# Optimization experiments

Hardware: AMD Instinct MI355X
Metric: run time of the kernel (lower is better)

The kernel has to match this reference:

```python
import jax, jax.numpy as jnp
import numpy as np
from jax import lax

B, T, C = 8, 1025, 512
HEADS = 8
CACHE = 256          # int(dim * cache_ratio)
CLS = 1
L = 256              # gr_cache memory length
H = W = 32           # sqrt(T - CLS)
EPS = 1e-5


def setup_inputs() -> dict:
    key = jax.random.key(0)
    ks = jax.random.split(key, 40)
    def w(k, shape, scale=0.02):
        return jax.random.normal(k, shape, dtype=jnp.float32) * scale
    inp = {}
    inp['x'] = jax.random.normal(ks[0], (B, T, C), dtype=jnp.float32)
    inp['gr_cache'] = jax.random.normal(ks[1], (1, L, CACHE), dtype=jnp.float32)
    # self-attention (dim=512) params, weights stored (in, out)
    inp['Wq1'] = w(ks[2], (C, C)); inp['bq1'] = jnp.zeros((C,), jnp.float32)
    inp['Wk1'] = w(ks[3], (C, C)); inp['bk1'] = jnp.zeros((C,), jnp.float32)
    inp['Wv1'] = w(ks[4], (C, C)); inp['bv1'] = jnp.zeros((C,), jnp.float32)
    inp['Wo1'] = w(ks[5], (C, C)); inp['bo1'] = jnp.zeros((C,), jnp.float32)
    # memory attention (dim=cache_dim=256) params
    inp['Wq2'] = w(ks[6], (CACHE, CACHE)); inp['bq2'] = jnp.zeros((CACHE,), jnp.float32)
    inp['Wk2'] = w(ks[7], (CACHE, CACHE)); inp['bk2'] = jnp.zeros((CACHE,), jnp.float32)
    inp['Wv2'] = w(ks[8], (CACHE, CACHE)); inp['bv2'] = jnp.zeros((CACHE,), jnp.float32)
    inp['Wo2'] = w(ks[9], (CACHE, CACHE)); inp['bo2'] = jnp.zeros((CACHE,), jnp.float32)
    # GRU-style gate linears: in = 2*cache_dim, out = cache_dim
    inp['Wr'] = w(ks[10], (2 * CACHE, CACHE)); inp['br'] = jnp.zeros((CACHE,), jnp.float32)
    inp['Wz'] = w(ks[11], (2 * CACHE, CACHE)); inp['bz'] = jnp.zeros((CACHE,), jnp.float32)
    inp['Wa'] = w(ks[12], (2 * CACHE, CACHE)); inp['ba'] = jnp.zeros((CACHE,), jnp.float32)
    # LayerNorm(cache_dim)
    inp['gamma'] = jnp.ones((CACHE,), jnp.float32)
    inp['beta'] = jnp.zeros((CACHE,), jnp.float32)
    # per-head gate logits, init to -1 as in the module
    inp['lam'] = jnp.full((HEADS,), -1.0, dtype=jnp.float32)
    # grouped conv pos-emb: Conv2d(512, 512, k=3, groups=CACHE) -> (O=512, I/g=2, 3, 3)
    inp['conv_w'] = w(ks[13], (C, C // CACHE, 3, 3))
    inp['conv_b'] = jnp.zeros((C,), jnp.float32)
    return inp


def _mha(q_in, kv_in, Wq, bq, Wk, bk, Wv, bv, Wo, bo):
    Bq, Tq, D = q_in.shape
    Tk = kv_in.shape[1]
    dh = D // HEADS
    q = (q_in @ Wq + bq).reshape(Bq, Tq, HEADS, dh)
    k = (kv_in @ Wk + bk).reshape(Bq, Tk, HEADS, dh)
    v = (kv_in @ Wv + bv).reshape(Bq, Tk, HEADS, dh)
    s = jnp.einsum('bqhd,bkhd->bhqk', q, k) * (1.0 / np.sqrt(dh)).astype(np.float32)
    a = jax.nn.softmax(s, axis=-1)
    o = jnp.einsum('bhqk,bkhd->bqhd', a, v).reshape(Bq, Tq, D)
    return o @ Wo + bo


def reference(x, gr_cache, Wq1, bq1, Wk1, bk1, Wv1, bv1, Wo1, bo1,
              Wq2, bq2, Wk2, bk2, Wv2, bv2, Wo2, bo2,
              Wr, br, Wz, bz, Wa, ba, gamma, beta, lam, conv_w, conv_b):
    B_, T_, C_ = x.shape
    # ---- spatial positional embedding (faithful to torch view->permute quirk) ----
    tok = x[:, CLS:, :].reshape(B_, H, W, C_).transpose(0, 3, 1, 2)   # (B, C, H, W)
    pos = lax.conv_general_dilated(tok, conv_w, (1, 1), 'SAME',
                                   feature_group_count=CACHE,
                                   dimension_numbers=('NCHW', 'OIHW', 'NCHW'))
    pos = pos + conv_b[None, :, None, None]
    pos = pos.reshape(B_, C_, T_ - CLS).transpose(0, 2, 1)            # (B, T-1, C)
    pos = jnp.concatenate([jnp.zeros((B_, CLS, C_), pos.dtype), pos], axis=1)
    # ---- self attention ----
    x_self = _mha(x, x, Wq1, bq1, Wk1, bk1, Wv1, bv1, Wo1, bo1)       # (B, T, C)
    x_self_h = x_self.reshape(B_, T_, HEADS, C_ // HEADS)
    # ---- GRU-style gated cache update ----
    gr = jnp.broadcast_to(gr_cache, (B_, L, CACHE))
    x_summary = x_self[:, :, :CACHE]
    idx = (jnp.arange(L) * T_) // L                                   # nearest interpolate T -> L
    x_summary = x_summary[:, idx, :]                                  # (B, L, CACHE)
    cat = jnp.concatenate([gr, x_summary], axis=-1)
    reset = jax.nn.sigmoid(cat @ Wr + br)
    z = jax.nn.sigmoid(cat @ Wz + bz)
    cat2 = jnp.concatenate([reset * gr, x_summary], axis=-1)
    add = jax.nn.gelu(cat2 @ Wa + ba, approximate=False)
    mu = add.mean(-1, keepdims=True)
    var = ((add - mu) ** 2).mean(-1, keepdims=True)
    add = (add - mu) / jnp.sqrt(var + EPS) * gamma + beta             # LayerNorm
    gr_new = z * add + (1.0 - z) * gr
    # ---- memory attention on first cache_dim channels ----
    x_mem = _mha(x[:, :, :CACHE], gr_new, Wq2, bq2, Wk2, bk2, Wv2, bv2, Wo2, bo2)
    x_mem = x_mem.reshape(B_, T_, HEADS, CACHE // HEADS)
    # ---- per-head alpha blend with zero-padded mem branch ----
    alpha = jax.nn.sigmoid(lam).reshape(1, 1, HEADS, 1)
    pad = jnp.zeros((B_, T_, HEADS, (C_ - CACHE) // HEADS), x.dtype)
    out = (alpha * jnp.concatenate([x_mem, pad], axis=-1)
           + (1.0 - alpha) * x_self_h).reshape(B_, T_, C_) + pos
    return out
```

## Files before the change

kernel.cpp:

```cpp
#include <hip/hip_runtime.h>
#include <math.h>

typedef unsigned short u16;
typedef unsigned int u32;
typedef __attribute__((ext_vector_type(8))) short short8;
typedef __attribute__((ext_vector_type(4))) short short4v;
typedef __attribute__((ext_vector_type(4))) float f32x4;

constexpr int Bc = 8;
constexpr int Tt = 1025;
constexpr int Cc = 512;
constexpr int Hn = 8;
constexpr int CA = 256;
constexpr int Ll = 256;

__device__ __forceinline__ u16 f2bf(float f) {
  u32 u = __builtin_bit_cast(u32, f);
  u = (u + 0x7FFFu + ((u >> 16) & 1u)) >> 16;
  return (u16)u;
}
__device__ __forceinline__ u32 pack2(float lo, float hi) {
  return (u32)f2bf(lo) | ((u32)f2bf(hi) << 16);
}

struct WC { const float* s; u16* d; int N; int tot; int kshift; };
struct WCP { WC w[11]; };

__global__ void wcast_k(WCP p) {
  const WC a = p.w[blockIdx.y];
  const int kmask = (1 << a.kshift) - 1;
  for (int idx = blockIdx.x * 256 + threadIdx.x; idx < a.tot; idx += gridDim.x * 256) {
    const int k = idx & kmask;
    const int n = idx >> a.kshift;
    a.d[idx] = f2bf(a.s[(size_t)k * a.N + n]);
  }
}

__global__ void xcast_k(const float* __restrict__ x, u16* __restrict__ xb, int n) {
  const int i = blockIdx.x * 256 + threadIdx.x;
  if (i < n) xb[i] = f2bf(x[i]);
}

enum { EP_NONE = 0, EP_SIGMOID = 1, EP_GELU = 2 };

template <int OUTBF, int ACT>
__global__ __launch_bounds__(256) void gemm_mfma(
    const u16* __restrict__ A, int lda,
    const u16* __restrict__ Wt,
    const float* __restrict__ bias,
    void* __restrict__ Cout,
    int M, int N, int K, float oscale)
{
  __shared__ u16 As[128][32];
  __shared__ u16 Bs[128][32];
  const int tid = threadIdx.x;
  const int m0 = blockIdx.y * 128, n0 = blockIdx.x * 128;
  const int ln = tid & 15, quad = (tid >> 4) & 3, wv = tid >> 6;
  const int wm = (wv & 1) * 64, wn = (wv >> 1) * 64;
  const int sr = tid >> 1;
  const int sk = (tid & 1) * 16;

  f32x4 zf = {0.f, 0.f, 0.f, 0.f};
  f32x4 acc[4][4];
  #pragma unroll
  for (int i = 0; i < 4; i++)
    #pragma unroll
    for (int j = 0; j < 4; j++) acc[i][j] = zf;

  const short8 z8 = {0, 0, 0, 0, 0, 0, 0, 0};

  for (int k0 = 0; k0 < K; k0 += 32) {
    const int gm = m0 + sr;
    short8 a0 = z8, a1 = z8;
    if (gm < M) {
      const u16* p = A + (size_t)gm * lda + k0 + sk;
      a0 = *(const short8*)p;
      a1 = *(const short8*)(p + 8);
    }
    *(short8*)&As[sr][sk] = a0;
    *(short8*)&As[sr][sk + 8] = a1;
    {
      const u16* q = Wt + (size_t)(n0 + sr) * K + k0 + sk;
      *(short8*)&Bs[sr][sk] = *(const short8*)q;
      *(short8*)&Bs[sr][sk + 8] = *(const short8*)(q + 8);
    }
    __syncthreads();

    short8 af[4], bf[4];
    #pragma unroll
    for (int i = 0; i < 4; i++) af[i] = *(const short8*)&As[wm + i * 16 + ln][quad * 8];
    #pragma unroll
    for (int j = 0; j < 4; j++) bf[j] = *(const short8*)&Bs[wn + j * 16 + ln][quad * 8];
    #pragma unroll
    for (int i = 0; i < 4; i++)
      #pragma unroll
      for (int j = 0; j < 4; j++)
        acc[i][j] = __builtin_amdgcn_mfma_f32_16x16x32_bf16(af[i], bf[j], acc[i][j], 0, 0, 0);
    __syncthreads();
  }

  float bj[4];
  #pragma unroll
  for (int j = 0; j < 4; j++) bj[j] = bias[n0 + wn + j * 16 + ln];

  #pragma unroll
  for (int i = 0; i < 4; i++) {
    #pragma unroll
    for (int r = 0; r < 4; r++) {
      const int gm = m0 + wm + i * 16 + quad * 4 + r;
      if (gm >= M) continue;
      #pragma unroll
      for (int j = 0; j < 4; j++) {
        float v = (acc[i][j][r] + bj[j]) * oscale;
        if (ACT == EP_SIGMOID)   v = 1.f / (1.f + __expf(-v));
        else if (ACT == EP_GELU) v = 0.5f * v * (1.f + erff(v * 0.70710678118654752f));
        const size_t off = (size_t)gm * N + n0 + wn + j * 16 + ln;
        if (OUTBF) ((u16*)Cout)[off] = f2bf(v);
        else       ((float*)Cout)[off] = v;
      }
    }
  }
}

template <int DH>
__global__ __launch_bounds__(128) void attn_mfma(
    const u16* __restrict__ Qp, const u16* __restrict__ Kp,
    const u16* __restrict__ Vp, u16* __restrict__ Op,
    int Tq, int Tk, int qbs, int kbs)
{
  constexpr int RS = Hn * DH;
  constexpr int KS = DH + 8;
  constexpr int VS = 40;
  constexpr int NC = DH / 32;
  constexpr int NM = DH / 16;

  __shared__ u16 Ks[32][KS];
  __shared__ u16 Vt[DH][VS];
  __shared__ u16 Pb[2][32][VS];

  const int b = blockIdx.y >> 3, h = blockIdx.y & 7;
  const int q0 = blockIdx.x * 64;
  const int tid = threadIdx.x;
  const int wv = tid >> 6;
  const int lane = tid & 63;
  const int ln = lane & 15, quad = lane >> 4;

  const u16* Qb = Qp + (size_t)b * qbs + h * DH;
  const u16* Kb = Kp + (size_t)b * kbs + h * DH;
  const u16* Vb = Vp + (size_t)b * kbs + h * DH;
  u16* Ob = Op + (size_t)b * qbs + h * DH;

  const short8 z8 = {0, 0, 0, 0, 0, 0, 0, 0};
  const f32x4 zf = {0.f, 0.f, 0.f, 0.f};

  short8 qf[2][NC];
  #pragma unroll
  for (int qs = 0; qs < 2; qs++) {
    const int gq = q0 + wv * 32 + qs * 16 + ln;
    #pragma unroll
    for (int c = 0; c < NC; c++) {
      if (gq < Tq) qf[qs][c] = *(const short8*)(Qb + (size_t)gq * RS + c * 32 + quad * 8);
      else         qf[qs][c] = z8;
    }
  }

  f32x4 oacc[2][NM];
  float lsum[2] = {0.f, 0.f};
  #pragma unroll
  for (int qs = 0; qs < 2; qs++)
    #pragma unroll
    for (int c = 0; c < NM; c++) oacc[qs][c] = zf;

  const int skk = tid >> 2;
  const int sd0 = (tid & 3) * (DH / 4);
  const int vd0 = (tid & 15) * (DH / 16);
  const int vk  = (tid >> 4) * 4;

  const int nit = (Tk + 31) >> 5;
  for (int it = 0; it < nit; it++) {
    const int k0 = it << 5;
    __syncthreads();
    {
      const int gk = k0 + skk;
      if (DH == 64) {
        short8 a = z8, b2 = z8;
        if (gk < Tk) {
          const u16* p = Kb + (size_t)gk * RS + sd0;
          a = *(const short8*)p;
          b2 = *(const short8*)(p + 8);
        }
        *(short8*)&Ks[skk][sd0] = a;
        *(short8*)&Ks[skk][sd0 + 8] = b2;
      } else {
        short8 a = z8;
        if (gk < Tk) a = *(const short8*)(Kb + (size_t)gk * RS + sd0);
        *(short8*)&Ks[skk][sd0] = a;
      }
    }
    {
      short4v vrow[4];
      #pragma unroll
      for (int i2 = 0; i2 < 4; i2++) {
        const int gk = k0 + vk + i2;
        short4v t = {0, 0, 0, 0};
        if (DH == 64) {
          if (gk < Tk) t = *(const short4v*)(Vb + (size_t)gk * RS + vd0);
        } else {
          if (gk < Tk) {
            ushort2 u = *(const ushort2*)(Vb + (size_t)gk * RS + vd0);
            t[0] = (short)u.x; t[1] = (short)u.y;
          }
        }
        vrow[i2] = t;
      }
      #pragma unroll
      for (int i = 0; i < DH / 16; i++) {
        short4v w = {vrow[0][i], vrow[1][i], vrow[2][i], vrow[3][i]};
        *(short4v*)&Vt[vd0 + i][vk] = w;
      }
    }
    __syncthreads();

    short8 kf[2][NC];
    #pragma unroll
    for (int kc = 0; kc < 2; kc++)
      #pragma unroll
      for (int c = 0; c < NC; c++)
        kf[kc][c] = *(const short8*)&Ks[kc * 16 + ln][c * 32 + quad * 8];

    #pragma unroll
    for (int qs = 0; qs < 2; qs++) {
      #pragma unroll
      for (int kc = 0; kc < 2; kc++) {
        f32x4 s = zf;
        #pragma unroll
        for (int c = 0; c < NC; c++)
          s = __builtin_amdgcn_mfma_f32_16x16x32_bf16(kf[kc][c], qf[qs][c], s, 0, 0, 0);
        float p[4];
        #pragma unroll
        for (int r = 0; r < 4; r++) {
          const int key = k0 + kc * 16 + quad * 4 + r;
          p[r] = (key < Tk) ? __expf(s[r]) : 0.f;
          lsum[qs] += p[r];
        }
        short4v w;
        ((u32*)&w)[0] = pack2(p[0], p[1]);
        ((u32*)&w)[1] = pack2(p[2], p[3]);
        *(short4v*)&Pb[wv][qs * 16 + ln][kc * 16 + quad * 4] = w;
      }
    }

    short8 pf2[2];
    #pragma unroll
    for (int qs = 0; qs < 2; qs++)
      pf2[qs] = *(const short8*)&Pb[wv][qs * 16 + ln][quad * 8];
    #pragma unroll
    for (int c = 0; c < NM; c++) {
      const short8 vf = *(const short8*)&Vt[c * 16 + ln][quad * 8];
      #pragma unroll
      for (int qs = 0; qs < 2; qs++)
        oacc[qs][c] = __builtin_amdgcn_mfma_f32_16x16x32_bf16(pf2[qs], vf, oacc[qs][c], 0, 0, 0);
    }
  }

  float lq[2];
  #pragma unroll
  for (int qs = 0; qs < 2; qs++) {
    float t = lsum[qs];
    t += __shfl_xor(t, 16);
    t += __shfl_xor(t, 32);
    lq[qs] = t;
  }
  #pragma unroll
  for (int qs = 0; qs < 2; qs++) {
    #pragma unroll
    for (int r = 0; r < 4; r++) {
      const float linv = 1.f / __shfl(lq[qs], quad * 4 + r);
      const int gq = q0 + wv * 32 + qs * 16 + quad * 4 + r;
      if (gq >= Tq) continue;
      #pragma unroll
      for (int c = 0; c < NM; c++)
        Ob[(size_t)gq * RS + c * 16 + ln] = f2bf(oacc[qs][c][r] * linv);
    }
  }
}

__global__ __launch_bounds__(256) void conv_combine(
    const float* __restrict__ x, const float* __restrict__ cw,
    const float* __restrict__ cb, const float* __restrict__ x_self,
    const float* __restrict__ x_mem, const float* __restrict__ lam,
    float* __restrict__ out)
{
  const int bh = blockIdx.x;
  const int b = bh >> 5, hh = bh & 31;
  const int c = (blockIdx.y << 8) + threadIdx.x;
  const int ci = c & ~1;
  const int dd = c & 63;
  const int h8 = c >> 6;
  const float alpha = 1.f / (1.f + __expf(-lam[h8]));
  const float bias = cb[c];

  float wgt[2][9];
  #pragma unroll
  for (int ch = 0; ch < 2; ch++)
    #pragma unroll
    for (int k = 0; k < 9; k++) wgt[ch][k] = cw[c * 18 + ch * 9 + k];

  const float* xrow[3];
  bool rv[3];
  #pragma unroll
  for (int r = 0; r < 3; r++) {
    const int h2 = hh + r - 1;
    rv[r] = (unsigned)h2 < 32u;
    xrow[r] = x + ((size_t)(b * Tt) + 1 + h2 * 32) * Cc + ci;
  }

  float2 win[3][3];
  #pragma unroll
  for (int r = 0; r < 3; r++) {
    win[r][0] = make_float2(0.f, 0.f);
    win[r][1] = rv[r] ? *(const float2*)(xrow[r]) : make_float2(0.f, 0.f);
  }

  const size_t bT = (size_t)b * Tt;
  for (int w = 0; w < 32; w++) {
    #pragma unroll
    for (int r = 0; r < 3; r++)
      win[r][2] = (rv[r] && w + 1 < 32) ? *(const float2*)(xrow[r] + (w + 1) * Cc)
                                        : make_float2(0.f, 0.f);
    float pos = bias;
    #pragma unroll
    for (int r = 0; r < 3; r++)
      #pragma unroll
      for (int col = 0; col < 3; col++) {
        pos += win[r][col].x * wgt[0][r * 3 + col];
        pos += win[r][col].y * wgt[1][r * 3 + col];
      }
    const size_t bt = bT + 1 + hh * 32 + w;
    const float mem = (dd < 32) ? x_mem[bt * 256 + h8 * 32 + dd] : 0.f;
    out[bt * 512 + c] = pos + alpha * mem + (1.f - alpha) * x_self[bt * 512 + c];
    #pragma unroll
    for (int r = 0; r < 3; r++) { win[r][0] = win[r][1]; win[r][1] = win[r][2]; }
  }

  if (hh == 0) {
    const float mem = (dd < 32) ? x_mem[bT * 256 + h8 * 32 + dd] : 0.f;
    out[bT * 512 + c] = alpha * mem + (1.f - alpha) * x_self[bT * 512 + c];
  }
}

__global__ void build_cat(const float* __restrict__ gr_cache,
                          const float* __restrict__ x_self,
                          u16* __restrict__ cat)
{
  const int idx = blockIdx.x * 256 + threadIdx.x;
  if (idx >= Bc * Ll * 512) return;
  const int k = idx & 511;
  const int bi = idx >> 9;
  const int i = bi & 255;
  const int b = bi >> 8;
  float v;
  if (k < 256) v = gr_cache[i * 256 + k];
  else         v = x_self[((size_t)(b * Tt + 4 * i)) * Cc + (k - 256)];
  cat[idx] = f2bf(v);
}

__global__ void build_cat2(const float* __restrict__ gr_cache,
                           const float* __restrict__ reset,
                           u16* __restrict__ cat)
{
  const int idx = blockIdx.x * 256 + threadIdx.x;
  if (idx >= Bc * Ll * 256) return;
  const int k = idx & 255;
  const int bi = idx >> 8;
  const int i = bi & 255;
  cat[(size_t)bi * 512 + k] = f2bf(gr_cache[i * 256 + k] * reset[idx]);
}

__device__ inline float block_sum256(float v, float* red)
{
  #pragma unroll
  for (int o = 32; o >= 1; o >>= 1) v += __shfl_down(v, o);
  const int wid = threadIdx.x >> 6;
  if ((threadIdx.x & 63) == 0) red[wid] = v;
  __syncthreads();
  const float t = red[0] + red[1] + red[2] + red[3];
  __syncthreads();
  return t;
}

__global__ __launch_bounds__(256) void ln_gate(
    const float* __restrict__ add_raw, const float* __restrict__ z,
    const float* __restrict__ gr_cache, const float* __restrict__ gamma,
    const float* __restrict__ beta, u16* __restrict__ gr_new)
{
  __shared__ float red[4];
  const int bi = blockIdx.x;
  const int i = bi & 255;
  const int c = threadIdx.x;
  const float v = add_raw[(size_t)bi * 256 + c];
  const float mu = block_sum256(v, red) * (1.f / 256.f);
  const float dv = v - mu;
  const float var = block_sum256(dv * dv, red) * (1.f / 256.f);
  const float nrm = dv * rsqrtf(var + 1e-5f) * gamma[c] + beta[c];
  const float zz = z[(size_t)bi * 256 + c];
  gr_new[(size_t)bi * 256 + c] = f2bf(zz * nrm + (1.f - zz) * gr_cache[i * 256 + c]);
}

extern "C" void kernel_launch(void* const* d_in, const int* in_sizes, int n_in,
                              void* d_out, int out_size, void* d_ws, size_t ws_size,
                              hipStream_t stream)
{
  const float* x        = (const float*)d_in[0];
  const float* gr_cache = (const float*)d_in[1];
  const float* Wq1 = (const float*)d_in[2];  const float* bq1 = (const float*)d_in[3];
  const float* Wk1 = (const float*)d_in[4];  const float* bk1 = (const float*)d_in[5];
  const float* Wv1 = (const float*)d_in[6];  const float* bv1 = (const float*)d_in[7];
  const float* Wo1 = (const float*)d_in[8];  const float* bo1 = (const float*)d_in[9];
  const float* Wq2 = (const float*)d_in[10]; const float* bq2 = (const float*)d_in[11];
  const float* Wk2 = (const float*)d_in[12]; const float* bk2 = (const float*)d_in[13];
  const float* Wv2 = (const float*)d_in[14]; const float* bv2 = (const float*)d_in[15];
  const float* Wo2 = (const float*)d_in[16]; const float* bo2 = (const float*)d_in[17];
  const float* Wr  = (const float*)d_in[18]; const float* br  = (const float*)d_in[19];
  const float* Wz  = (const float*)d_in[20]; const float* bz  = (const float*)d_in[21];
  const float* Wa  = (const float*)d_in[22]; const float* ba  = (const float*)d_in[23];
  const float* gamma = (const float*)d_in[24];
  const float* beta  = (const float*)d_in[25];
  const float* lam   = (const float*)d_in[26];
  const float* conv_w = (const float*)d_in[27];
  const float* conv_b = (const float*)d_in[28];
  float* out = (float*)d_out;

  const int M1 = Bc * Tt;
  const int M2 = Bc * Ll;
  const size_t BTC = (size_t)Bc * Tt * Cc;
  const size_t BLA = (size_t)Bc * Ll * CA;
  const size_t BL2 = (size_t)Bc * Ll * 512;

  char* W = (char*)d_ws;
  u16*   xb     = (u16*)(W + 0);
  u16*   q1     = (u16*)(W + 8396800);
  u16*   k1     = (u16*)(W + 16793600);
  u16*   v1     = (u16*)(W + 25190400);
  u16*   att1   = (u16*)(W + 33587200);
  float* x_self = (float*)(W + 41984000);
  u16*   wtb    = (u16*)(W + 58777600);
  u16*   cat    = (u16*)(W + 8396800);
  float* rg     = (float*)(W + 10493952);
  float* zg     = (float*)(W + 12591104);
  float* addr_  = (float*)(W + 14688256);
  u16*   gr_new = (u16*)(W + 16785408);
  u16*   k2     = (u16*)(W + 17833984);
  u16*   v2     = (u16*)(W + 18882560);
  u16*   q2     = (u16*)(W + 19931136);
  u16*   att2   = (u16*)(W + 24129536);
  float* x_mem  = (float*)(W + 28327936);

  u16* Wq1t = wtb + 0;       u16* Wk1t = wtb + 262144;  u16* Wv1t = wtb + 524288;
  u16* Wo1t = wtb + 786432;  u16* Wrt  = wtb + 1048576; u16* Wzt  = wtb + 1179648;
  u16* Wat  = wtb + 1310720; u16* Wq2t = wtb + 1441792; u16* Wk2t = wtb + 1507328;
  u16* Wv2t = wtb + 1572864; u16* Wo2t = wtb + 1638400;

  const dim3 blk(256);
  const int ew_btc = (int)((BTC + 255) / 256);

  {
    WCP p;
    const float* ws_[11] = {Wq1, Wk1, Wv1, Wo1, Wr, Wz, Wa, Wq2, Wk2, Wv2, Wo2};
    u16* wd_[11] = {Wq1t, Wk1t, Wv1t, Wo1t, Wrt, Wzt, Wat, Wq2t, Wk2t, Wv2t, Wo2t};
    const int Kk[11] = {512,512,512,512,512,512,512,256,256,256,256};
    const int Nn[11] = {512,512,512,512,256,256,256,256,256,256,256};
    for (int i = 0; i < 11; i++) {
      p.w[i].s = ws_[i]; p.w[i].d = wd_[i]; p.w[i].N = Nn[i];
      p.w[i].tot = Kk[i] * Nn[i];
      p.w[i].kshift = (Kk[i] == 512) ? 9 : 8;
    }
    wcast_k<<<dim3(64, 11), blk, 0, stream>>>(p);
  }
  xcast_k<<<ew_btc, blk, 0, stream>>>(x, xb, (int)BTC);

  const dim3 g512(4, 65), g256m1(2, 65), g256m2(2, 16);
  gemm_mfma<1, EP_NONE><<<g512, blk, 0, stream>>>(xb, 512, Wq1t, bq1, q1, M1, 512, 512, 0.125f);
  gemm_mfma<1, EP_NONE><<<g512, blk, 0, stream>>>(xb, 512, Wk1t, bk1, k1, M1, 512, 512, 1.f);
  gemm_mfma<1, EP_NONE><<<g512, blk, 0, stream>>>(xb, 512, Wv1t, bv1, v1, M1, 512, 512, 1.f);
  attn_mfma<64><<<dim3(17, 64), dim3(128), 0, stream>>>(q1, k1, v1, att1, Tt, Tt,
                                                        Tt * 512, Tt * 512);
  gemm_mfma<0, EP_NONE><<<g512, blk, 0, stream>>>(att1, 512, Wo1t, bo1, x_self, M1, 512, 512, 1.f);

  build_cat<<<(int)((BL2 + 255) / 256), blk, 0, stream>>>(gr_cache, x_self, cat);
  gemm_mfma<0, EP_SIGMOID><<<g256m2, blk, 0, stream>>>(cat, 512, Wrt, br, rg, M2, 256, 512, 1.f);
  gemm_mfma<0, EP_SIGMOID><<<g256m2, blk, 0, stream>>>(cat, 512, Wzt, bz, zg, M2, 256, 512, 1.f);
  build_cat2<<<(int)((BLA + 255) / 256), blk, 0, stream>>>(gr_cache, rg, cat);
  gemm_mfma<0, EP_GELU><<<g256m2, blk, 0, stream>>>(cat, 512, Wat, ba, addr_, M2, 256, 512, 1.f);
  ln_gate<<<M2, blk, 0, stream>>>(addr_, zg, gr_cache, gamma, beta, gr_new);

  gemm_mfma<1, EP_NONE><<<g256m1, blk, 0, stream>>>(xb, 512, Wq2t, bq2, q2, M1, 256, 256,
                                                    0.17677669529663689f);
  gemm_mfma<1, EP_NONE><<<g256m2, blk, 0, stream>>>(gr_new, 256, Wk2t, bk2, k2, M2, 256, 256, 1.f);
  gemm_mfma<1, EP_NONE><<<g256m2, blk, 0, stream>>>(gr_new, 256, Wv2t, bv2, v2, M2, 256, 256, 1.f);
  attn_mfma<32><<<dim3(17, 64), dim3(128), 0, stream>>>(q2, k2, v2, att2, Tt, Ll,
                                                        Tt * 256, Ll * 256);
  gemm_mfma<0, EP_NONE><<<g256m1, blk, 0, stream>>>(att2, 256, Wo2t, bo2, x_mem, M1, 256, 256, 1.f);

  conv_combine<<<dim3(Bc * 32, 2), blk, 0, stream>>>(x, conv_w, conv_b, x_self,
                                                     x_mem, lam, out);
}
```

Measured before the change: 407.1 us.

## Swizzle attention LDS layouts, use exp2 with folded log2e, cheaper bf16 packing

Replaces the padded shared-memory tiles for K, transposed V and P in the attention kernel with XOR-swizzled unpadded layouts to avoid bank conflicts. Folds log2(e) into the Q projection scale so the softmax can use a native exp2. Adds a fast path that skips bounds checks on full key tiles. Swaps the round-to-nearest-even bf16 packing for a byte-permute with add-0x8000 rounding. The new packing rounds ties differently, which may shift results slightly.

Result: faster. 397.2 us (-2.4%).

```diff
diff --git a/kernel.cpp b/kernel.cpp
--- a/kernel.cpp
+++ b/kernel.cpp
@@ -14,13 +14,21 @@
 constexpr int CA = 256;
 constexpr int Ll = 256;
 
+#if __has_builtin(__builtin_amdgcn_exp2f)
+#define EXP2F __builtin_amdgcn_exp2f
+#else
+#define EXP2F exp2f
+#endif
+
 __device__ __forceinline__ u16 f2bf(float f) {
   u32 u = __builtin_bit_cast(u32, f);
   u = (u + 0x7FFFu + ((u >> 16) & 1u)) >> 16;
   return (u16)u;
 }
-__device__ __forceinline__ u32 pack2(float lo, float hi) {
-  return (u32)f2bf(lo) | ((u32)f2bf(hi) << 16);
+__device__ __forceinline__ u32 pack2f(float lo, float hi) {
+  const u32 a = __builtin_bit_cast(u32, hi) + 0x8000u;
+  const u32 b = __builtin_bit_cast(u32, lo) + 0x8000u;
+  return __builtin_amdgcn_perm(a, b, 0x07060302u);
 }
 
 struct WC { const float* s; u16* d; int N; int tot; int kshift; };
@@ -129,14 +137,13 @@
     int Tq, int Tk, int qbs, int kbs)
 {
   constexpr int RS = Hn * DH;
-  constexpr int KS = DH + 8;
-  constexpr int VS = 40;
+  constexpr int MK = DH / 8 - 1;
   constexpr int NC = DH / 32;
   constexpr int NM = DH / 16;
 
-  __shared__ u16 Ks[32][KS];
-  __shared__ u16 Vt[DH][VS];
-  __shared__ u16 Pb[2][32][VS];
+  __shared__ u16 Ks[32 * DH];
+  __shared__ u16 Vt[DH * 32];
+  __shared__ u16 Pb[2 * 32 * 32];
 
   const int b = blockIdx.y >> 3, h = blockIdx.y & 7;
   const int q0 = blockIdx.x * 64;
@@ -171,42 +178,46 @@
     #pragma unroll
     for (int c = 0; c < NM; c++) oacc[qs][c] = zf;
 
-  const int skk = tid >> 2;
-  const int sd0 = (tid & 3) * (DH / 4);
-  const int vd0 = (tid & 15) * (DH / 16);
-  const int vk  = (tid >> 4) * 4;
-
+  const int nfull = Tk >> 5;
   const int nit = (Tk + 31) >> 5;
+
   for (int it = 0; it < nit; it++) {
     const int k0 = it << 5;
+    const bool full = (it < nfull);
     __syncthreads();
+
     {
-      const int gk = k0 + skk;
+      const int r = tid >> 2;
+      const int gk = k0 + r;
       if (DH == 64) {
+        const u16* p = Kb + (size_t)gk * RS + (tid & 3) * 16;
         short8 a = z8, b2 = z8;
-        if (gk < Tk) {
-          const u16* p = Kb + (size_t)gk * RS + sd0;
-          a = *(const short8*)p;
-          b2 = *(const short8*)(p + 8);
-        }
-        *(short8*)&Ks[skk][sd0] = a;
-        *(short8*)&Ks[skk][sd0 + 8] = b2;
+        if (full || gk < Tk) { a = *(const short8*)p; b2 = *(const short8*)(p + 8); }
+        const int g0 = (((tid & 3) * 2) ^ (r & 7));
+        const int g1 = (((tid & 3) * 2 + 1) ^ (r & 7));
+        *(short8*)&Ks[r * 64 + g0 * 8] = a;
+        *(short8*)&Ks[r * 64 + g1 * 8] = b2;
       } else {
+        const u16* p = Kb + (size_t)gk * RS + (tid & 3) * 8;
         short8 a = z8;
-        if (gk < Tk) a = *(const short8*)(Kb + (size_t)gk * RS + sd0);
-        *(short8*)&Ks[skk][sd0] = a;
+        if (full || gk < Tk) a = *(const short8*)p;
+        const int g0 = ((tid & 3) ^ (r & 3));
+        *(short8*)&Ks[r * 32 + g0 * 8] = a;
       }
     }
     {
+      const int vd0 = (tid & 15) * (DH / 16);
+      const int vk = (tid >> 4) * 4;
+      const int gb = vk >> 3, off = vk & 7;
       short4v vrow[4];
       #pragma unroll
       for (int i2 = 0; i2 < 4; i2++) {
         const int gk = k0 + vk + i2;
         short4v t = {0, 0, 0, 0};
         if (DH == 64) {
-          if (gk < Tk) t = *(const short4v*)(Vb + (size_t)gk * RS + vd0);
+          if (full || gk < Tk) t = *(const short4v*)(Vb + (size_t)gk * RS + vd0);
         } else {
-          if (gk < Tk) {
+          if (full || gk < Tk) {
             ushort2 u = *(const ushort2*)(Vb + (size_t)gk * RS + vd0);
             t[0] = (short)u.x; t[1] = (short)u.y;
           }
@@ -215,18 +226,24 @@
       }
       #pragma unroll
       for (int i = 0; i < DH / 16; i++) {
+        const int d = vd0 + i;
+        const int h2 = (d ^ (d >> 3)) & 3;
         short4v w = {vrow[0][i], vrow[1][i], vrow[2][i], vrow[3][i]};
-        *(short4v*)&Vt[vd0 + i][vk] = w;
+        *(short4v*)&Vt[d * 32 + ((gb ^ h2) << 3) + off] = w;
       }
     }
     __syncthreads();
 
     short8 kf[2][NC];
     #pragma unroll
-    for (int kc = 0; kc < 2; kc++)
-      #pragma unroll
-      for (int c = 0; c < NC; c++)
-        kf[kc][c] = *(const short8*)&Ks[kc * 16 + ln][c * 32 + quad * 8];
+    for (int kc = 0; kc < 2; kc++) {
+      const int r = kc * 16 + ln;
+      #pragma unroll
+      for (int c = 0; c < NC; c++) {
+        const int g = (4 * c + quad) ^ (r & MK);
+        kf[kc][c] = *(const short8*)&Ks[r * DH + g * 8];
+      }
+    }
 
     #pragma unroll
     for (int qs = 0; qs < 2; qs++) {
@@ -236,27 +253,38 @@
         #pragma unroll
         for (int c = 0; c < NC; c++)
           s = __builtin_amdgcn_mfma_f32_16x16x32_bf16(kf[kc][c], qf[qs][c], s, 0, 0, 0);
-        float p[4];
-        #pragma unroll
-        for (int r = 0; r < 4; r++) {
-          const int key = k0 + kc * 16 + quad * 4 + r;
-          p[r] = (key < Tk) ? __expf(s[r]) : 0.f;
-          lsum[qs] += p[r];
+        float p0, p1, p2, p3;
+        if (full) {
+          p0 = EXP2F(s[0]); p1 = EXP2F(s[1]); p2 = EXP2F(s[2]); p3 = EXP2F(s[3]);
+        } else {
+          const int kb = k0 + kc * 16 + quad * 4;
+          p0 = (kb + 0 < Tk) ? EXP2F(s[0]) : 0.f;
+          p1 = (kb + 1 < Tk) ? EXP2F(s[1]) : 0.f;
+          p2 = (kb + 2 < Tk) ? EXP2F(s[2]) : 0.f;
+          p3 = (kb + 3 < Tk) ? EXP2F(s[3]) : 0.f;
         }
-        short4v w;
-        ((u32*)&w)[0] = pack2(p[0], p[1]);
-        ((u32*)&w)[1] = pack2(p[2], p[3]);
-        *(short4v*)&Pb[wv][qs * 16 + ln][kc * 16 + quad * 4] = w;
+        lsum[qs] += (p0 + p1) + (p2 + p3);
+        short4v pw;
+        ((u32*)&pw)[0] = pack2f(p0, p1);
+        ((u32*)&pw)[1] = pack2f(p2, p3);
+        const int q = qs * 16 + ln;
+        const int g = ((kc * 2 + (quad >> 1)) ^ (ln & 3)) & 3;
+        *(short4v*)&Pb[wv * 1024 + q * 32 + (g << 3) + (quad & 1) * 4] = pw;
       }
     }
 
     short8 pf2[2];
     #pragma unroll
-    for (int qs = 0; qs < 2; qs++)
-      pf2[qs] = *(const short8*)&Pb[wv][qs * 16 + ln][quad * 8];
+    for (int qs = 0; qs < 2; qs++) {
+      const int q = qs * 16 + ln;
+      const int g = quad ^ (ln & 3);
+      pf2[qs] = *(const short8*)&Pb[wv * 1024 + q * 32 + g * 8];
+    }
     #pragma unroll
     for (int c = 0; c < NM; c++) {
-      const short8 vf = *(const short8*)&Vt[c * 16 + ln][quad * 8];
+      const int d = c * 16 + ln;
+      const int g = quad ^ ((d ^ (d >> 3)) & 3);
+      const short8 vf = *(const short8*)&Vt[d * 32 + g * 8];
       #pragma unroll
       for (int qs = 0; qs < 2; qs++)
         oacc[qs][c] = __builtin_amdgcn_mfma_f32_16x16x32_bf16(pf2[qs], vf, oacc[qs][c], 0, 0, 0);
@@ -480,7 +508,8 @@
   xcast_k<<<ew_btc, blk, 0, stream>>>(x, xb, (int)BTC);
 
   const dim3 g512(4, 65), g256m1(2, 65), g256m2(2, 16);
-  gemm_mfma<1, EP_NONE><<<g512, blk, 0, stream>>>(xb, 512, Wq1t, bq1, q1, M1, 512, 512, 0.125f);
+  gemm_mfma<1, EP_NONE><<<g512, blk, 0, stream>>>(xb, 512, Wq1t, bq1, q1, M1, 512, 512,
+                                                  0.18033688011112042f);
   gemm_mfma<1, EP_NONE><<<g512, blk, 0, stream>>>(xb, 512, Wk1t, bk1, k1, M1, 512, 512, 1.f);
   gemm_mfma<1, EP_NONE><<<g512, blk, 0, stream>>>(xb, 512, Wv1t, bv1, v1, M1, 512, 512, 1.f);
   attn_mfma<64><<<dim3(17, 64), dim3(128), 0, stream>>>(q1, k1, v1, att1, Tt, Tt,
@@ -495,7 +524,7 @@
   ln_gate<<<M2, blk, 0, stream>>>(addr_, zg, gr_cache, gamma, beta, gr_new);
 
   gemm_mfma<1, EP_NONE><<<g256m1, blk, 0, stream>>>(xb, 512, Wq2t, bq2, q2, M1, 256, 256,
-                                                    0.17677669529663689f);
+                                                    0.25503490664918414f);
   gemm_mfma<1, EP_NONE><<<g256m2, blk, 0, stream>>>(gr_new, 256, Wk2t, bk2, k2, M2, 256, 256, 1.f);
   gemm_mfma<1, EP_NONE><<<g256m2, blk, 0, stream>>>(gr_new, 256, Wv2t, bv2, v2, M2, 256, 256, 1.f);
   attn_mfma<32><<<dim3(17, 64), dim3(128), 0, stream>>>(q2, k2, v2, att2, Tt, Ll,
```
